# Kernel optimization log

Measured on AMD Instinct MI355X. Metric: run time of the kernel, lower is better.

Reference implementation:

```python
import jax, jax.numpy as jnp
import numpy as np

T = 8192
F = 128   # feature_size
H = 2048  # hidden_size
PRED_LEN = 12  # pred_length (fc_out head exists in module but is unused in forward)


def setup_inputs() -> dict:
    key = jax.random.key(0)
    ks = jax.random.split(key, 10)
    s_ih = 1.0 / np.sqrt(H)
    inp = {
        "x": jax.random.normal(ks[0], (T, F), dtype=jnp.float32),
        # PyTorch nn.LSTM params, gate order [i, f, g, o]
        "W_ih": jax.random.uniform(ks[1], (4 * H, F), jnp.float32, -s_ih, s_ih),
        "W_hh": jax.random.uniform(ks[2], (4 * H, H), jnp.float32, -s_ih, s_ih),
        "b_ih": jax.random.uniform(ks[3], (4 * H,), jnp.float32, -s_ih, s_ih),
        "b_hh": jax.random.uniform(ks[4], (4 * H,), jnp.float32, -s_ih, s_ih),
        # self.linear: Linear(H, H)
        "W_lin": jax.random.uniform(ks[5], (H, H), jnp.float32, -s_ih, s_ih),
        "b_lin": jax.random.uniform(ks[6], (H,), jnp.float32, -s_ih, s_ih),
        # self.one_out: Linear(H, 2)
        "W_out": jax.random.uniform(ks[7], (2, H), jnp.float32, -s_ih, s_ih),
        "b_out": jax.random.uniform(ks[8], (2,), jnp.float32, -s_ih, s_ih),
    }
    return inp


def _lstm_last_h(x, W_ih, W_hh, b_ih, b_hh):
    # x: [T, F]; returns final hidden state h: [H]
    # Precompute input projections for all timesteps: [T, 4H]
    x_proj = x @ W_ih.T + (b_ih + b_hh)

    def step(carry, xp):
        h, c = carry
        gates = xp + h @ W_hh.T  # [4H]
        i = jax.nn.sigmoid(gates[0 * H:1 * H])
        f = jax.nn.sigmoid(gates[1 * H:2 * H])
        g = jnp.tanh(gates[2 * H:3 * H])
        o = jax.nn.sigmoid(gates[3 * H:4 * H])
        c = f * c + i * g
        h = o * jnp.tanh(c)
        return (h, c), None

    h0 = jnp.zeros((H,), x.dtype)
    c0 = jnp.zeros((H,), x.dtype)
    (h, _), _ = jax.lax.scan(step, (h0, c0), x_proj)
    return h


def reference(x, W_ih, W_hh, b_ih, b_hh, W_lin, b_lin, W_out, b_out):
    h = _lstm_last_h(x, W_ih, W_hh, b_ih, b_hh)        # [H]
    y = h @ W_lin.T + b_lin                            # [H]
    y = y @ W_out.T + b_out                            # [2]
    return y.reshape(1, 1, 2)                          # matches torch (1,1,2)
```

## Files before the change

kernel.cpp:

```cpp
#include <hip/hip_runtime.h>


#define H      2048
#define TSTEPS 8192
#define FEAT   128
#define NBLK   256
#define NTHR   512

typedef float vf4 __attribute__((ext_vector_type(4)));
typedef float vf2 __attribute__((ext_vector_type(2)));
typedef unsigned long long u64;
typedef unsigned int u32;

__device__ __forceinline__ float sigm(float xv) {
  return __builtin_amdgcn_rcpf(1.0f + __expf(-xv));
}
__device__ __forceinline__ float tanh_(float xv) {
  return 1.0f - 2.0f * __builtin_amdgcn_rcpf(__expf(2.0f * xv) + 1.0f);
}

__device__ __forceinline__ u64 aload64(const u64* p) {
  return __hip_atomic_load(p, __ATOMIC_RELAXED, __HIP_MEMORY_SCOPE_AGENT);
}
__device__ __forceinline__ u32 aload32(const u32* p) {
  return __hip_atomic_load(p, __ATOMIC_RELAXED, __HIP_MEMORY_SCOPE_AGENT);
}
__device__ __forceinline__ void astoref(float* p, float v) {
  __hip_atomic_store(p, v, __ATOMIC_RELAXED, __HIP_MEMORY_SCOPE_AGENT);
}
__device__ __forceinline__ void astoreu(u32* p, u32 v) {
  __hip_atomic_store(p, v, __ATOMIC_RELAXED, __HIP_MEMORY_SCOPE_AGENT);
}

#define DECLG(g) vf4 w##g##_0, w##g##_1, w##g##_2, w##g##_3, \
                     w##g##_4, w##g##_5, w##g##_6, w##g##_7; \
                 vf2 wih##g; float bias##g; float acc##g;

#define LOADG(g) { \
  const int row_ = (g) * H + j; \
  const float* wr_ = W_hh + (long)row_ * H; \
  w##g##_0 = *(const vf4*)(wr_ + 4*(ln      )); \
  w##g##_1 = *(const vf4*)(wr_ + 4*(ln +  64)); \
  w##g##_2 = *(const vf4*)(wr_ + 4*(ln + 128)); \
  w##g##_3 = *(const vf4*)(wr_ + 4*(ln + 192)); \
  w##g##_4 = *(const vf4*)(wr_ + 4*(ln + 256)); \
  w##g##_5 = *(const vf4*)(wr_ + 4*(ln + 320)); \
  w##g##_6 = *(const vf4*)(wr_ + 4*(ln + 384)); \
  w##g##_7 = *(const vf4*)(wr_ + 4*(ln + 448)); \
  wih##g  = *(const vf2*)(W_ih + (long)row_ * FEAT + 2*ln); \
  bias##g = b_ih[row_] + b_hh[row_]; }

#define PIN(g) asm volatile("" : \
  "+v"(w##g##_0), "+v"(w##g##_1), "+v"(w##g##_2), "+v"(w##g##_3), \
  "+v"(w##g##_4), "+v"(w##g##_5), "+v"(w##g##_6), "+v"(w##g##_7), \
  "+v"(wih##g), "+v"(bias##g));

#define LDSREAD(k, ldsrow) \
  const vf4 hv##k = *(const vf4*)&(ldsrow)[4*(ln + 64*(k))];

#define FMA_G(g, c) \
  acc##g = __builtin_fmaf(w##g##_##c.x, h4_.x, acc##g); \
  acc##g = __builtin_fmaf(w##g##_##c.y, h4_.y, acc##g); \
  acc##g = __builtin_fmaf(w##g##_##c.z, h4_.z, acc##g); \
  acc##g = __builtin_fmaf(w##g##_##c.w, h4_.w, acc##g);

#define FMA_C(c) { const vf4 h4_ = hv##c; \
  FMA_G(0, c) FMA_G(1, c) FMA_G(2, c) FMA_G(3, c) }

#define REDUCE(g) { float a_ = acc##g; \
  a_ += __shfl_xor(a_, 1);  a_ += __shfl_xor(a_, 2);  a_ += __shfl_xor(a_, 4); \
  a_ += __shfl_xor(a_, 8);  a_ += __shfl_xor(a_, 16); a_ += __shfl_xor(a_, 32); \
  acc##g = a_ + bias##g; }

__device__ __forceinline__ void poll_and_stage(const u32* __restrict__ slots,
                                               const float* __restrict__ hsrc,
                                               int tgt,
                                               float* __restrict__ ldsrow,
                                               int wv, int ln) {
  const u32* sp = slots + wv * 32 + (ln & 31);
  const bool act = (ln < 32);
  int v0 = act ? (int)aload32(sp) : 0x7fffffff;
  int v1 = act ? (int)aload32(sp) : 0x7fffffff;
  while (!__all(v0 >= tgt)) {
    __builtin_amdgcn_s_sleep(1);
    v0 = v1;
    v1 = act ? (int)aload32(sp) : 0x7fffffff;
  }
  const int base = wv * 256 + 4 * ln;
  const u64* hp = (const u64*)(hsrc + base);
  const u64 d0 = aload64(hp);
  const u64 d1 = aload64(hp + 1);
  vf4 hv;
  hv.x = __uint_as_float((u32)d0);
  hv.y = __uint_as_float((u32)(d0 >> 32));
  hv.z = __uint_as_float((u32)d1);
  hv.w = __uint_as_float((u32)(d1 >> 32));
  *(vf4*)&ldsrow[base] = hv;
}

__global__ __launch_bounds__(NTHR, 2)
void lstm_persist(const float* __restrict__ x,
                  const float* __restrict__ W_ih,
                  const float* __restrict__ W_hh,
                  const float* __restrict__ b_ih,
                  const float* __restrict__ b_hh,
                  const float* __restrict__ W_lin,
                  const float* __restrict__ b_lin,
                  const float* __restrict__ W_out,
                  const float* __restrict__ b_out,
                  float* __restrict__ out,
                  float* __restrict__ ws)
{
  const int tid = threadIdx.x;
  const int b   = blockIdx.x;
  const int wv  = tid >> 6;
  const int ln  = tid & 63;

  float* hbuf0 = ws;
  float* hbuf1 = ws + H;
  u32*   slots = (u32*)(ws + 2 * H);

  __shared__ __align__(16) float h_lds[2][H];

  *(vf4*)&h_lds[0][4 * tid] = (vf4)(0.0f);

  const int j = b * 8 + wv;
  DECLG(0) DECLG(1) DECLG(2) DECLG(3)
  LOADG(0) LOADG(1) LOADG(2) LOADG(3)
  PIN(0) PIN(1) PIN(2) PIN(3)

  __syncthreads();

  float cst = 0.0f;

  #pragma unroll 1
  for (int t = 0; t < TSTEPS; ++t) {
    const vf2 xr = *(const vf2*)(x + (long)t * FEAT + 2 * ln);
    float* ldsrow = h_lds[t & 1];

    if (t > 0)
      poll_and_stage(slots, (t & 1) ? hbuf1 : hbuf0, t, ldsrow, wv, ln);
    __syncthreads();

    LDSREAD(0, ldsrow) LDSREAD(1, ldsrow) LDSREAD(2, ldsrow) LDSREAD(3, ldsrow)
    LDSREAD(4, ldsrow) LDSREAD(5, ldsrow) LDSREAD(6, ldsrow) LDSREAD(7, ldsrow)

    acc0 = wih0.x * xr.x + wih0.y * xr.y;
    acc1 = wih1.x * xr.x + wih1.y * xr.y;
    acc2 = wih2.x * xr.x + wih2.y * xr.y;
    acc3 = wih3.x * xr.x + wih3.y * xr.y;

    FMA_C(0) FMA_C(1) FMA_C(2) FMA_C(3)
    FMA_C(4) FMA_C(5) FMA_C(6) FMA_C(7)

    REDUCE(0) REDUCE(1) REDUCE(2) REDUCE(3)

    const float iv = sigm(acc0);
    const float fv = sigm(acc1);
    const float gv = tanh_(acc2);
    const float ov = sigm(acc3);
    cst = fv * cst + iv * gv;
    const float hval = ov * tanh_(cst);

    if (ln == 0)
      astoref((((t + 1) & 1) ? hbuf1 : hbuf0) + j, hval);

    __syncthreads();
    if (tid == 0)
      astoreu(slots + b, (u32)(t + 1));
  }

  {
    float* ldsrow = h_lds[0];
    poll_and_stage(slots, hbuf0, TSTEPS, ldsrow, wv, ln);
    __syncthreads();

    float a0 = 0.0f;
    const float* wl = W_lin + (long)j * H;
    #pragma unroll
    for (int k = 0; k < 8; ++k) {
      const vf4 h4 = *(const vf4*)&ldsrow[4 * (ln + 64 * k)];
      const vf4 u  = *(const vf4*)(wl + 4 * (ln + 64 * k));
      a0 += u.x * h4.x + u.y * h4.y + u.z * h4.z + u.w * h4.w;
    }
    a0 += __shfl_xor(a0, 1);  a0 += __shfl_xor(a0, 2);  a0 += __shfl_xor(a0, 4);
    a0 += __shfl_xor(a0, 8);  a0 += __shfl_xor(a0, 16); a0 += __shfl_xor(a0, 32);

    if (ln == 0)
      astoref(hbuf1 + j, a0 + b_lin[j]);
    __syncthreads();
    if (tid == 0)
      astoreu(slots + b, (u32)(TSTEPS + 1));
  }

  if (b == 0 && wv == 0) {
    const u32* sp = slots + 4 * ln;
    int v0 = (int)aload32(sp + 0), v1 = (int)aload32(sp + 1);
    int v2 = (int)aload32(sp + 2), v3 = (int)aload32(sp + 3);
    const int tgt = TSTEPS + 1;
    while (!__all((v0 >= tgt) & (v1 >= tgt) & (v2 >= tgt) & (v3 >= tgt))) {
      __builtin_amdgcn_s_sleep(1);
      if (v0 < tgt) v0 = (int)aload32(sp + 0);
      if (v1 < tgt) v1 = (int)aload32(sp + 1);
      if (v2 < tgt) v2 = (int)aload32(sp + 2);
      if (v3 < tgt) v3 = (int)aload32(sp + 3);
    }
    float p0 = 0.0f, p1 = 0.0f;
    #pragma unroll
    for (int k = 0; k < 16; ++k) {
      const u64 d  = aload64((const u64*)hbuf1 + ln + 64 * k);
      const int c  = 2 * (ln + 64 * k);
      const float ylo = __uint_as_float((u32)d);
      const float yhi = __uint_as_float((u32)(d >> 32));
      p0 = __builtin_fmaf(W_out[c],         ylo, p0);
      p0 = __builtin_fmaf(W_out[c + 1],     yhi, p0);
      p1 = __builtin_fmaf(W_out[H + c],     ylo, p1);
      p1 = __builtin_fmaf(W_out[H + c + 1], yhi, p1);
    }
    p0 += __shfl_xor(p0, 1);  p0 += __shfl_xor(p0, 2);  p0 += __shfl_xor(p0, 4);
    p0 += __shfl_xor(p0, 8);  p0 += __shfl_xor(p0, 16); p0 += __shfl_xor(p0, 32);
    p1 += __shfl_xor(p1, 1);  p1 += __shfl_xor(p1, 2);  p1 += __shfl_xor(p1, 4);
    p1 += __shfl_xor(p1, 8);  p1 += __shfl_xor(p1, 16); p1 += __shfl_xor(p1, 32);
    if (ln == 0) {
      out[0] = p0 + b_out[0];
      out[1] = p1 + b_out[1];
    }
  }
}

extern "C" void kernel_launch(void* const* d_in, const int* in_sizes, int n_in,
                              void* d_out, int out_size, void* d_ws, size_t ws_size,
                              hipStream_t stream) {
  const float* x     = (const float*)d_in[0];
  const float* W_ih  = (const float*)d_in[1];
  const float* W_hh  = (const float*)d_in[2];
  const float* b_ih  = (const float*)d_in[3];
  const float* b_hh  = (const float*)d_in[4];
  const float* W_lin = (const float*)d_in[5];
  const float* b_lin = (const float*)d_in[6];
  const float* W_out = (const float*)d_in[7];
  const float* b_out = (const float*)d_in[8];

  lstm_persist<<<dim3(NBLK), dim3(NTHR), 0, stream>>>(
      x, W_ih, W_hh, b_ih, b_hh, W_lin, b_lin, W_out, b_out,
      (float*)d_out, (float*)d_ws);
}
```

Baseline: 32.23 ms.

## Tag hidden-state entries with step numbers so slot publishing skips the block barrier

Each hidden-state entry is now stored as a 64-bit word holding the value plus its timestep tag. Consumers, after polling the per-block slots, spin until every tag they read reaches the target step. Because of this, each block can publish its slot from wave 0 right after its own stores drain, instead of waiting on a block-wide barrier first. This shortens the critical path of the per-step grid synchronisation, at the cost of twice as many bytes per hidden-state read and an extra spin loop on the data itself.

```diff
diff --git a/kernel.cpp b/kernel.cpp
--- a/kernel.cpp
+++ b/kernel.cpp
@@ -25,11 +25,16 @@
 __device__ __forceinline__ u32 aload32(const u32* p) {
   return __hip_atomic_load(p, __ATOMIC_RELAXED, __HIP_MEMORY_SCOPE_AGENT);
 }
-__device__ __forceinline__ void astoref(float* p, float v) {
+__device__ __forceinline__ void astore64(u64* p, u64 v) {
   __hip_atomic_store(p, v, __ATOMIC_RELAXED, __HIP_MEMORY_SCOPE_AGENT);
 }
 __device__ __forceinline__ void astoreu(u32* p, u32 v) {
   __hip_atomic_store(p, v, __ATOMIC_RELAXED, __HIP_MEMORY_SCOPE_AGENT);
+}
+__device__ __forceinline__ int  tag_of(u64 d) { return (int)(u32)(d >> 32); }
+__device__ __forceinline__ float val_of(u64 d) { return __uint_as_float((u32)d); }
+__device__ __forceinline__ u64  pack(int tag, float v) {
+  return ((u64)(u32)tag << 32) | (u64)__float_as_uint(v);
 }
 
 #define DECLG(g) vf4 w##g##_0, w##g##_1, w##g##_2, w##g##_3, \
@@ -73,7 +78,7 @@
   acc##g = a_ + bias##g; }
 
 __device__ __forceinline__ void poll_and_stage(const u32* __restrict__ slots,
-                                               const float* __restrict__ hsrc,
+                                               const u64* __restrict__ hq_par,
                                                int tgt,
                                                float* __restrict__ ldsrow,
                                                int wv, int ln) {
@@ -87,14 +92,24 @@
     v1 = act ? (int)aload32(sp) : 0x7fffffff;
   }
   const int base = wv * 256 + 4 * ln;
-  const u64* hp = (const u64*)(hsrc + base);
-  const u64 d0 = aload64(hp);
-  const u64 d1 = aload64(hp + 1);
+  const u64* hp = hq_par + base;
+  u64 d0 = aload64(hp + 0);
+  u64 d1 = aload64(hp + 1);
+  u64 d2 = aload64(hp + 2);
+  u64 d3 = aload64(hp + 3);
+  while (!__all((tag_of(d0) >= tgt) & (tag_of(d1) >= tgt) &
+                (tag_of(d2) >= tgt) & (tag_of(d3) >= tgt))) {
+    __builtin_amdgcn_s_sleep(1);
+    if (tag_of(d0) < tgt) d0 = aload64(hp + 0);
+    if (tag_of(d1) < tgt) d1 = aload64(hp + 1);
+    if (tag_of(d2) < tgt) d2 = aload64(hp + 2);
+    if (tag_of(d3) < tgt) d3 = aload64(hp + 3);
+  }
   vf4 hv;
-  hv.x = __uint_as_float((u32)d0);
-  hv.y = __uint_as_float((u32)(d0 >> 32));
-  hv.z = __uint_as_float((u32)d1);
-  hv.w = __uint_as_float((u32)(d1 >> 32));
+  hv.x = val_of(d0);
+  hv.y = val_of(d1);
+  hv.z = val_of(d2);
+  hv.w = val_of(d3);
   *(vf4*)&ldsrow[base] = hv;
 }
 
@@ -116,9 +131,8 @@
   const int wv  = tid >> 6;
   const int ln  = tid & 63;
 
-  float* hbuf0 = ws;
-  float* hbuf1 = ws + H;
-  u32*   slots = (u32*)(ws + 2 * H);
+  u64* hq    = (u64*)ws;
+  u32* slots = (u32*)(ws + 4 * H);
 
   __shared__ __align__(16) float h_lds[2][H];
 
@@ -139,7 +153,7 @@
     float* ldsrow = h_lds[t & 1];
 
     if (t > 0)
-      poll_and_stage(slots, (t & 1) ? hbuf1 : hbuf0, t, ldsrow, wv, ln);
+      poll_and_stage(slots, hq + (t & 1) * H, t, ldsrow, wv, ln);
     __syncthreads();
 
     LDSREAD(0, ldsrow) LDSREAD(1, ldsrow) LDSREAD(2, ldsrow) LDSREAD(3, ldsrow)
@@ -163,16 +177,45 @@
     const float hval = ov * tanh_(cst);
 
     if (ln == 0)
-      astoref((((t + 1) & 1) ? hbuf1 : hbuf0) + j, hval);
-
-    __syncthreads();
-    if (tid == 0)
-      astoreu(slots + b, (u32)(t + 1));
+      astore64(hq + ((t + 1) & 1) * H + j, pack(t + 1, hval));
+    if (wv == 0) {
+      asm volatile("s_waitcnt vmcnt(0)" ::: "memory");
+      if (ln == 0)
+        astoreu(slots + b, (u32)(t + 1));
+    }
+    __syncthreads();
   }
 
   {
+    const u32* sp = slots + 4 * ln;
+    int v0 = (int)aload32(sp + 0), v1 = (int)aload32(sp + 1);
+    int v2 = (int)aload32(sp + 2), v3 = (int)aload32(sp + 3);
+    while (!__all((v0 >= TSTEPS) & (v1 >= TSTEPS) &
+                  (v2 >= TSTEPS) & (v3 >= TSTEPS))) {
+      __builtin_amdgcn_s_sleep(1);
+      if (v0 < TSTEPS) v0 = (int)aload32(sp + 0);
+      if (v1 < TSTEPS) v1 = (int)aload32(sp + 1);
+      if (v2 < TSTEPS) v2 = (int)aload32(sp + 2);
+      if (v3 < TSTEPS) v3 = (int)aload32(sp + 3);
+    }
     float* ldsrow = h_lds[0];
-    poll_and_stage(slots, hbuf0, TSTEPS, ldsrow, wv, ln);
+    const int base = wv * 256 + 4 * ln;
+    const u64* hp = hq + base;
+    u64 d0 = aload64(hp + 0);
+    u64 d1 = aload64(hp + 1);
+    u64 d2 = aload64(hp + 2);
+    u64 d3 = aload64(hp + 3);
+    while (!__all((tag_of(d0) >= TSTEPS) & (tag_of(d1) >= TSTEPS) &
+                  (tag_of(d2) >= TSTEPS) & (tag_of(d3) >= TSTEPS))) {
+      __builtin_amdgcn_s_sleep(1);
+      if (tag_of(d0) < TSTEPS) d0 = aload64(hp + 0);
+      if (tag_of(d1) < TSTEPS) d1 = aload64(hp + 1);
+      if (tag_of(d2) < TSTEPS) d2 = aload64(hp + 2);
+      if (tag_of(d3) < TSTEPS) d3 = aload64(hp + 3);
+    }
+    vf4 hv;
+    hv.x = val_of(d0); hv.y = val_of(d1); hv.z = val_of(d2); hv.w = val_of(d3);
+    *(vf4*)&ldsrow[base] = hv;
     __syncthreads();
 
     float a0 = 0.0f;
@@ -187,7 +230,7 @@
     a0 += __shfl_xor(a0, 8);  a0 += __shfl_xor(a0, 16); a0 += __shfl_xor(a0, 32);
 
     if (ln == 0)
-      astoref(hbuf1 + j, a0 + b_lin[j]);
+      astore64(hq + H + j, pack(TSTEPS + 1, a0 + b_lin[j]));
     __syncthreads();
     if (tid == 0)
       astoreu(slots + b, (u32)(TSTEPS + 1));
@@ -207,15 +250,12 @@
     }
     float p0 = 0.0f, p1 = 0.0f;
     #pragma unroll
-    for (int k = 0; k < 16; ++k) {
-      const u64 d  = aload64((const u64*)hbuf1 + ln + 64 * k);
-      const int c  = 2 * (ln + 64 * k);
-      const float ylo = __uint_as_float((u32)d);
-      const float yhi = __uint_as_float((u32)(d >> 32));
-      p0 = __builtin_fmaf(W_out[c],         ylo, p0);
-      p0 = __builtin_fmaf(W_out[c + 1],     yhi, p0);
-      p1 = __builtin_fmaf(W_out[H + c],     ylo, p1);
-      p1 = __builtin_fmaf(W_out[H + c + 1], yhi, p1);
+    for (int k = 0; k < 32; ++k) {
+      const u64 d  = aload64(hq + H + ln + 64 * k);
+      const float y = val_of(d);
+      const int c  = ln + 64 * k;
+      p0 = __builtin_fmaf(W_out[c],     y, p0);
+      p1 = __builtin_fmaf(W_out[H + c], y, p1);
     }
     p0 += __shfl_xor(p0, 1);  p0 += __shfl_xor(p0, 2);  p0 += __shfl_xor(p0, 4);
     p0 += __shfl_xor(p0, 8);  p0 += __shfl_xor(p0, 16); p0 += __shfl_xor(p0, 32);
```

Result: slower. 44.36 ms (+37.6%).

## Replace flag-and-buffer handoff with per-consumer tagged mailboxes

Applied to the files above, without the earlier changes.

Adds a kernel in which each block writes its 8 new hidden values, packed with a step tag as 64-bit words, into a separate mailbox for every consumer block. Consumers poll their own mailbox row and read value and readiness in the same load. This removes the separate slot-flag poll followed by a second data load, and the barrier before the flag store. In exchange every block issues 256x more global stores per step and needs a 2x256x256x8 u64 workspace, falling back to the old kernel when the workspace is too small.

```diff
diff --git a/kernel.cpp b/kernel.cpp
--- a/kernel.cpp
+++ b/kernel.cpp
@@ -30,6 +30,14 @@
 }
 __device__ __forceinline__ void astoreu(u32* p, u32 v) {
   __hip_atomic_store(p, v, __ATOMIC_RELAXED, __HIP_MEMORY_SCOPE_AGENT);
+}
+__device__ __forceinline__ void astore64(u64* p, u64 v) {
+  __hip_atomic_store(p, v, __ATOMIC_RELAXED, __HIP_MEMORY_SCOPE_AGENT);
+}
+__device__ __forceinline__ int  tag_of(u64 d) { return (int)(u32)(d >> 32); }
+__device__ __forceinline__ float val_of(u64 d) { return __uint_as_float((u32)d); }
+__device__ __forceinline__ u64  pack(int tag, float v) {
+  return ((u64)(u32)tag << 32) | (u64)__float_as_uint(v);
 }
 
 #define DECLG(g) vf4 w##g##_0, w##g##_1, w##g##_2, w##g##_3, \
@@ -71,6 +79,165 @@
   a_ += __shfl_xor(a_, 1);  a_ += __shfl_xor(a_, 2);  a_ += __shfl_xor(a_, 4); \
   a_ += __shfl_xor(a_, 8);  a_ += __shfl_xor(a_, 16); a_ += __shfl_xor(a_, 32); \
   acc##g = a_ + bias##g; }
+
+
+__device__ __forceinline__ void mbox_poll_stage(const u64* __restrict__ mrow,
+                                                int tgt,
+                                                float* __restrict__ ldsrow,
+                                                int wv, int ln) {
+  const u64* hp = mrow + (((wv << 5) + (ln >> 1)) << 3) + ((ln & 1) << 2);
+  u64 d0 = aload64(hp + 0);
+  u64 d1 = aload64(hp + 1);
+  u64 d2 = aload64(hp + 2);
+  u64 d3 = aload64(hp + 3);
+  while (!__all((tag_of(d0) >= tgt) & (tag_of(d1) >= tgt) &
+                (tag_of(d2) >= tgt) & (tag_of(d3) >= tgt))) {
+    __builtin_amdgcn_s_sleep(1);
+    if (tag_of(d0) < tgt) d0 = aload64(hp + 0);
+    if (tag_of(d1) < tgt) d1 = aload64(hp + 1);
+    if (tag_of(d2) < tgt) d2 = aload64(hp + 2);
+    if (tag_of(d3) < tgt) d3 = aload64(hp + 3);
+  }
+  vf4 hv;
+  hv.x = val_of(d0);
+  hv.y = val_of(d1);
+  hv.z = val_of(d2);
+  hv.w = val_of(d3);
+  *(vf4*)&ldsrow[wv * 256 + 4 * ln] = hv;
+}
+
+__global__ __launch_bounds__(NTHR, 2)
+void lstm_mbox(const float* __restrict__ x,
+               const float* __restrict__ W_ih,
+               const float* __restrict__ W_hh,
+               const float* __restrict__ b_ih,
+               const float* __restrict__ b_hh,
+               const float* __restrict__ W_lin,
+               const float* __restrict__ b_lin,
+               const float* __restrict__ W_out,
+               const float* __restrict__ b_out,
+               float* __restrict__ out,
+               float* __restrict__ ws)
+{
+  const int tid = threadIdx.x;
+  const int b   = blockIdx.x;
+  const int wv  = tid >> 6;
+  const int ln  = tid & 63;
+
+  u64* mbox = (u64*)ws;
+
+  __shared__ __align__(16) float h_lds[2][H];
+  __shared__ __align__(16) float hshare[8];
+
+  *(vf4*)&h_lds[0][4 * tid] = (vf4)(0.0f);
+
+  const int j = b * 8 + wv;
+  DECLG(0) DECLG(1) DECLG(2) DECLG(3)
+  LOADG(0) LOADG(1) LOADG(2) LOADG(3)
+  PIN(0) PIN(1) PIN(2) PIN(3)
+
+  __syncthreads();
+
+  const int cc = tid >> 1;
+  const int hf = tid & 1;
+
+  float cst = 0.0f;
+
+  #pragma unroll 1
+  for (int t = 0; t < TSTEPS; ++t) {
+    const vf2 xr = *(const vf2*)(x + (long)t * FEAT + 2 * ln);
+    float* ldsrow = h_lds[t & 1];
+
+    if (t > 0)
+      mbox_poll_stage(mbox + (((long)(t & 1) * NBLK + b) * NBLK << 3),
+                      t, ldsrow, wv, ln);
+    __syncthreads();
+
+    LDSREAD(0, ldsrow) LDSREAD(1, ldsrow) LDSREAD(2, ldsrow) LDSREAD(3, ldsrow)
+    LDSREAD(4, ldsrow) LDSREAD(5, ldsrow) LDSREAD(6, ldsrow) LDSREAD(7, ldsrow)
+
+    acc0 = wih0.x * xr.x + wih0.y * xr.y;
+    acc1 = wih1.x * xr.x + wih1.y * xr.y;
+    acc2 = wih2.x * xr.x + wih2.y * xr.y;
+    acc3 = wih3.x * xr.x + wih3.y * xr.y;
+
+    FMA_C(0) FMA_C(1) FMA_C(2) FMA_C(3)
+    FMA_C(4) FMA_C(5) FMA_C(6) FMA_C(7)
+
+    REDUCE(0) REDUCE(1) REDUCE(2) REDUCE(3)
+
+    const float iv = sigm(acc0);
+    const float fv = sigm(acc1);
+    const float gv = tanh_(acc2);
+    const float ov = sigm(acc3);
+    cst = fv * cst + iv * gv;
+    const float hval = ov * tanh_(cst);
+
+    if (ln == 0) hshare[wv] = hval;
+    __syncthreads();
+    {
+      u64* ep = mbox + ((((long)((t + 1) & 1) * NBLK + cc) * NBLK + b) << 3)
+                     + (hf << 2);
+      const int tg = t + 1;
+      astore64(ep + 0, pack(tg, hshare[hf * 4 + 0]));
+      astore64(ep + 1, pack(tg, hshare[hf * 4 + 1]));
+      astore64(ep + 2, pack(tg, hshare[hf * 4 + 2]));
+      astore64(ep + 3, pack(tg, hshare[hf * 4 + 3]));
+    }
+  }
+
+  {
+    float* ldsrow = h_lds[0];
+    mbox_poll_stage(mbox + ((long)b * NBLK << 3), TSTEPS, ldsrow, wv, ln);
+    __syncthreads();
+
+    float a0 = 0.0f;
+    const float* wl = W_lin + (long)j * H;
+    #pragma unroll
+    for (int k = 0; k < 8; ++k) {
+      const vf4 h4 = *(const vf4*)&ldsrow[4 * (ln + 64 * k)];
+      const vf4 u  = *(const vf4*)(wl + 4 * (ln + 64 * k));
+      a0 += u.x * h4.x + u.y * h4.y + u.z * h4.z + u.w * h4.w;
+    }
+    a0 += __shfl_xor(a0, 1);  a0 += __shfl_xor(a0, 2);  a0 += __shfl_xor(a0, 4);
+    a0 += __shfl_xor(a0, 8);  a0 += __shfl_xor(a0, 16); a0 += __shfl_xor(a0, 32);
+
+    if (ln == 0) hshare[wv] = a0 + b_lin[j];
+    __syncthreads();
+    if (tid < 2) {
+      u64* ep = mbox + ((((long)NBLK + 0) * NBLK + b) << 3) + (tid << 2);
+      astore64(ep + 0, pack(TSTEPS + 1, hshare[tid * 4 + 0]));
+      astore64(ep + 1, pack(TSTEPS + 1, hshare[tid * 4 + 1]));
+      astore64(ep + 2, pack(TSTEPS + 1, hshare[tid * 4 + 2]));
+      astore64(ep + 3, pack(TSTEPS + 1, hshare[tid * 4 + 3]));
+    }
+  }
+
+  if (b == 0) {
+    mbox_poll_stage(mbox + ((long)NBLK * NBLK << 3), TSTEPS + 1,
+                    h_lds[1], wv, ln);
+    __syncthreads();
+    if (wv == 0) {
+      float p0 = 0.0f, p1 = 0.0f;
+      #pragma unroll
+      for (int k = 0; k < 32; ++k) {
+        const float y = h_lds[1][ln + 64 * k];
+        p0 = __builtin_fmaf(W_out[ln + 64 * k],     y, p0);
+        p1 = __builtin_fmaf(W_out[H + ln + 64 * k], y, p1);
+      }
+      p0 += __shfl_xor(p0, 1);  p0 += __shfl_xor(p0, 2);  p0 += __shfl_xor(p0, 4);
+      p0 += __shfl_xor(p0, 8);  p0 += __shfl_xor(p0, 16); p0 += __shfl_xor(p0, 32);
+      p1 += __shfl_xor(p1, 1);  p1 += __shfl_xor(p1, 2);  p1 += __shfl_xor(p1, 4);
+      p1 += __shfl_xor(p1, 8);  p1 += __shfl_xor(p1, 16); p1 += __shfl_xor(p1, 32);
+      if (ln == 0) {
+        out[0] = p0 + b_out[0];
+        out[1] = p1 + b_out[1];
+      }
+    }
+  }
+  asm volatile("s_waitcnt vmcnt(0)" ::: "memory");
+}
+
 
 __device__ __forceinline__ void poll_and_stage(const u32* __restrict__ slots,
                                                const float* __restrict__ hsrc,
@@ -241,7 +408,14 @@
   const float* W_out = (const float*)d_in[7];
   const float* b_out = (const float*)d_in[8];
 
-  lstm_persist<<<dim3(NBLK), dim3(NTHR), 0, stream>>>(
-      x, W_ih, W_hh, b_ih, b_hh, W_lin, b_lin, W_out, b_out,
-      (float*)d_out, (float*)d_ws);
-}
+  const size_t need = (size_t)2 * NBLK * NBLK * 8 * sizeof(u64);
+  if (ws_size >= need) {
+    lstm_mbox<<<dim3(NBLK), dim3(NTHR), 0, stream>>>(
+        x, W_ih, W_hh, b_ih, b_hh, W_lin, b_lin, W_out, b_out,
+        (float*)d_out, (float*)d_ws);
+  } else {
+    lstm_persist<<<dim3(NBLK), dim3(NTHR), 0, stream>>>(
+        x, W_ih, W_hh, b_ih, b_hh, W_lin, b_lin, W_out, b_out,
+        (float*)d_out, (float*)d_ws);
+  }
+}
```

New measurement: 71.77 ms. 123% more time.
